# Optimization experiments

Hardware: AMD Instinct MI355X
Metric: run time of the kernel (lower is better)

Reference implementation:

```python
import math
import jax, jax.numpy as jnp
import numpy as np

B, CH3, T = 64, 192, 2048  # B = batch*heads, CH3 = 3*head_dim

def setup_inputs() -> dict:
    key = jax.random.key(0)
    qkv = jax.random.normal(key, (B, CH3, T), dtype=jnp.float32)
    return {"qkv": qkv}

def reference(qkv):
    ch = qkv.shape[1] // 3
    q, k, v = jnp.split(qkv, 3, axis=1)  # each [B, ch, T]
    scale = 1.0 / math.sqrt(math.sqrt(ch))
    # scores [B, T(query), S(key)]
    weight = jnp.einsum('bct,bcs->bts', q * scale, k * scale)
    weight = jax.nn.softmax(weight.astype(jnp.float32), axis=-1).astype(weight.dtype)
    return jnp.einsum('bts,bcs->bct', weight, v)
```

## Files before the change

### kernel.cpp

```cpp
#include <hip/hip_runtime.h>
#include <hip/hip_bf16.h>


#define DHEAD 64
#define TLEN  2048
#define NB    64
#define BQ    256
#define BK    64
#define LDA   72
#define LDT   65

typedef short s16x8 __attribute__((ext_vector_type(8)));
typedef float f32x4 __attribute__((ext_vector_type(4)));
typedef unsigned short u16x4 __attribute__((ext_vector_type(4)));
typedef unsigned short u16x8 __attribute__((ext_vector_type(8)));

__device__ __forceinline__ unsigned short f2bf(float f) {
    unsigned int u = __float_as_uint(f);
    u += 0x7fffu + ((u >> 16) & 1u);
    return (unsigned short)(u >> 16);
}

__device__ __forceinline__ unsigned int cvt_pk_bf16(float a, float b) {
    return (unsigned int)f2bf(a) | ((unsigned int)f2bf(b) << 16);
}

__global__ __launch_bounds__(256)
void prep_qk(const float* __restrict__ qkv, unsigned short* __restrict__ ws) {
    __shared__ float T32[64 * LDT];
    const int tile = blockIdx.x, tensor = blockIdx.y, b = blockIdx.z;
    const int tid = threadIdx.x;
    const float* src = qkv + ((size_t)b * 3 + tensor) * DHEAD * TLEN + tile * 64;
    unsigned short* dst = ws + (size_t)tensor * NB * DHEAD * TLEN
                        + (size_t)b * DHEAD * TLEN + (size_t)tile * 64 * DHEAD;
    {
        int c = tid >> 4, t4 = (tid & 15) * 4;
        #pragma unroll
        for (int rr = 0; rr < 4; ++rr, c += 16) {
            float4 f = *(const float4*)(src + c * TLEN + t4);
            T32[(t4 + 0) * LDT + c] = f.x;
            T32[(t4 + 1) * LDT + c] = f.y;
            T32[(t4 + 2) * LDT + c] = f.z;
            T32[(t4 + 3) * LDT + c] = f.w;
        }
    }
    __syncthreads();
    #pragma unroll
    for (int rep = 0; rep < 2; ++rep) {
        int idx = rep * 256 + tid;
        int t = idx >> 3, j = idx & 7;
        const float* row = &T32[t * LDT + j * 8];
        union { u16x8 v; unsigned int u[4]; } o;
        o.u[0] = cvt_pk_bf16(row[0], row[1]);
        o.u[1] = cvt_pk_bf16(row[2], row[3]);
        o.u[2] = cvt_pk_bf16(row[4], row[5]);
        o.u[3] = cvt_pk_bf16(row[6], row[7]);
        *(u16x8*)(dst + t * DHEAD + j * 8) = o.v;
    }
}

__global__ __launch_bounds__(256)
void prep_v(const float* __restrict__ qkv, unsigned short* __restrict__ ws) {
    const int tile = blockIdx.x, b = blockIdx.y;
    const int tid = threadIdx.x;
    const float* src = qkv + ((size_t)b * 3 + 2) * DHEAD * TLEN + tile * 256;
    unsigned short* dst = ws + (size_t)2 * NB * DHEAD * TLEN
                        + (size_t)b * DHEAD * TLEN + tile * 256;
    int c = tid >> 5, t8 = (tid & 31) * 8;
    #pragma unroll
    for (int rr = 0; rr < 8; ++rr, c += 8) {
        float4 f0 = *(const float4*)(src + c * TLEN + t8);
        float4 f1 = *(const float4*)(src + c * TLEN + t8 + 4);
        union { u16x8 v; unsigned int u[4]; } o;
        o.u[0] = cvt_pk_bf16(f0.x, f0.y);
        o.u[1] = cvt_pk_bf16(f0.z, f0.w);
        o.u[2] = cvt_pk_bf16(f1.x, f1.y);
        o.u[3] = cvt_pk_bf16(f1.z, f1.w);
        *(u16x8*)(dst + c * TLEN + t8) = o.v;
    }
}

__device__ __forceinline__ void loadkv(const unsigned short* kt, const unsigned short* vd,
                                       int s0, u16x8 kc[2], u16x8 vc[2], int tid) {
    #pragma unroll
    for (int r = 0; r < 2; ++r) {
        int id = tid + r * 256;
        kc[r] = *(const u16x8*)(kt + (size_t)s0 * DHEAD + id * 8);
        vc[r] = *(const u16x8*)(vd + (size_t)(id >> 3) * TLEN + s0 + (id & 7) * 8);
    }
}

__device__ __forceinline__ void stage(unsigned short* K, unsigned short* V,
                                      const u16x8 kc[2], const u16x8 vc[2], int tid) {
    #pragma unroll
    for (int r = 0; r < 2; ++r) {
        int id = tid + r * 256;
        *(u16x8*)(&K[(id >> 3) * LDA + (id & 7) * 8]) = kc[r];
        *(u16x8*)(&V[(id >> 3) * LDA + (id & 7) * 8]) = vc[r];
    }
}

__device__ __forceinline__ void compute_tile(const unsigned short* Ks, const unsigned short* Vs,
                                             unsigned short* Pw,
                                             const s16x8 (&qf)[4][2], f32x4 (&acco)[4][4],
                                             float (&lp)[4], int quad, int c16) {
    f32x4 accs[4][4];
    #pragma unroll
    for (int i = 0; i < 4; ++i)
        #pragma unroll
        for (int j = 0; j < 4; ++j) accs[i][j] = f32x4{0.f, 0.f, 0.f, 0.f};
    #pragma unroll
    for (int kk = 0; kk < 2; ++kk)
        #pragma unroll
        for (int st = 0; st < 4; ++st) {
            s16x8 ka = *(const s16x8*)(&Ks[(st * 16 + c16) * LDA + kk * 32 + quad * 8]);
            #pragma unroll
            for (int ts = 0; ts < 4; ++ts)
                accs[st][ts] = __builtin_amdgcn_mfma_f32_16x16x32_bf16(ka, qf[ts][kk], accs[st][ts], 0, 0, 0);
        }

    #pragma unroll
    for (int st = 0; st < 4; ++st)
        #pragma unroll
        for (int ts = 0; ts < 4; ++ts) {
            f32x4 v = accs[st][ts];
            float e0 = __expf(v[0] * 0.125f);
            float e1 = __expf(v[1] * 0.125f);
            float e2 = __expf(v[2] * 0.125f);
            float e3 = __expf(v[3] * 0.125f);
            lp[ts] += (e0 + e1) + (e2 + e3);
            union { u16x4 v4; unsigned int u[2]; } p;
            p.u[0] = cvt_pk_bf16(e0, e1);
            p.u[1] = cvt_pk_bf16(e2, e3);
            *(u16x4*)(&Pw[(ts * 16 + c16) * LDA + st * 16 + quad * 4]) = p.v4;
        }

    #pragma unroll
    for (int kk = 0; kk < 2; ++kk) {
        s16x8 pb[4];
        #pragma unroll
        for (int ts = 0; ts < 4; ++ts)
            pb[ts] = *(const s16x8*)(&Pw[(ts * 16 + c16) * LDA + kk * 32 + quad * 8]);
        #pragma unroll
        for (int cst = 0; cst < 4; ++cst) {
            s16x8 va = *(const s16x8*)(&Vs[(cst * 16 + c16) * LDA + kk * 32 + quad * 8]);
            #pragma unroll
            for (int ts = 0; ts < 4; ++ts)
                acco[cst][ts] = __builtin_amdgcn_mfma_f32_16x16x32_bf16(va, pb[ts], acco[cst][ts], 0, 0, 0);
        }
    }
}

__global__ __launch_bounds__(256, 2)
void attn(const unsigned short* __restrict__ ws, float* __restrict__ out) {
    __shared__ alignas(16) unsigned short Ks2[2][64 * LDA];
    __shared__ alignas(16) unsigned short Vs2[2][64 * LDA];
    __shared__ alignas(16) unsigned short Pt[4][64 * LDA];

    const int tid  = threadIdx.x;
    const int wave = tid >> 6;
    const int lane = tid & 63;
    const int quad = lane >> 4;
    const int c16  = lane & 15;

    const int b  = blockIdx.y;
    const int t0 = blockIdx.x * BQ;

    const unsigned short* qt = ws + (size_t)b * DHEAD * TLEN + (size_t)(t0 + wave * 64) * DHEAD;
    const unsigned short* kt = ws + (size_t)NB * DHEAD * TLEN + (size_t)b * DHEAD * TLEN;
    const unsigned short* vd = ws + (size_t)2 * NB * DHEAD * TLEN + (size_t)b * DHEAD * TLEN;

    s16x8 qf[4][2];
    #pragma unroll
    for (int ts = 0; ts < 4; ++ts)
        #pragma unroll
        for (int kk = 0; kk < 2; ++kk)
            qf[ts][kk] = *(const s16x8*)(qt + (size_t)(ts * 16 + c16) * DHEAD + kk * 32 + quad * 8);

    f32x4 acco[4][4];
    #pragma unroll
    for (int i = 0; i < 4; ++i)
        #pragma unroll
        for (int j = 0; j < 4; ++j) acco[i][j] = f32x4{0.f, 0.f, 0.f, 0.f};
    float lp[4] = {0.f, 0.f, 0.f, 0.f};

    unsigned short* Pw = Pt[wave];

    u16x8 kcA[2], vcA[2], kcB[2], vcB[2];
    loadkv(kt, vd, 0, kcA, vcA, tid);
    loadkv(kt, vd, BK, kcB, vcB, tid);

    for (int it = 0; it < TLEN / BK; it += 2) {
        stage(Ks2[0], Vs2[0], kcA, vcA, tid);
        __syncthreads();
        if (it + 2 < TLEN / BK) loadkv(kt, vd, (it + 2) * BK, kcA, vcA, tid);
        compute_tile(Ks2[0], Vs2[0], Pw, qf, acco, lp, quad, c16);

        stage(Ks2[1], Vs2[1], kcB, vcB, tid);
        __syncthreads();
        if (it + 3 < TLEN / BK) loadkv(kt, vd, (it + 3) * BK, kcB, vcB, tid);
        compute_tile(Ks2[1], Vs2[1], Pw, qf, acco, lp, quad, c16);
    }

    float rinv[4];
    #pragma unroll
    for (int ts = 0; ts < 4; ++ts) {
        float l = lp[ts];
        l += __shfl_xor(l, 16);
        l += __shfl_xor(l, 32);
        rinv[ts] = 1.0f / l;
    }

    float* ob = out + (size_t)b * DHEAD * TLEN + t0 + wave * 64;
    #pragma unroll
    for (int cst = 0; cst < 4; ++cst)
        #pragma unroll
        for (int ts = 0; ts < 4; ++ts)
            #pragma unroll
            for (int r = 0; r < 4; ++r)
                ob[(size_t)(cst * 16 + quad * 4 + r) * TLEN + ts * 16 + c16] = acco[cst][ts][r] * rinv[ts];
}

extern "C" void kernel_launch(void* const* d_in, const int* in_sizes, int n_in,
                              void* d_out, int out_size, void* d_ws, size_t ws_size,
                              hipStream_t stream) {
    const float* qkv = (const float*)d_in[0];
    unsigned short* ws = (unsigned short*)d_ws;
    float* out = (float*)d_out;
    prep_qk<<<dim3(TLEN / 64, 2, NB), 256, 0, stream>>>(qkv, ws);
    prep_v<<<dim3(TLEN / 256, NB), 256, 0, stream>>>(qkv, ws);
    attn<<<dim3(TLEN / BQ, NB), 256, 0, stream>>>(ws, out);
}
```

Baseline: 271.6 us.

## Switch attention to fp16 MFMA with pre-scaled Q/K and single-buffered LDS

Converts the workspace and MFMA operands from bf16 to fp16, using the hardware pkrtz conversion in place of the software round-to-nearest bf16 routine. The score scale is folded into Q and K during prep so the per-element multiply before exp disappears. The attention loop drops the double-buffered K/V LDS tiles for a single buffer with an extra barrier per tile, which shrinks LDS use but exposes more synchronisation. fp16 carries less range than bf16, and the exp values are not max-subtracted, so large scores risk overflowing.

```diff
diff --git a/kernel.cpp b/kernel.cpp
--- a/kernel.cpp
+++ b/kernel.cpp
@@ -1,5 +1,4 @@
 #include <hip/hip_runtime.h>
-#include <hip/hip_bf16.h>
 
 
 #define DHEAD 64
@@ -10,29 +9,28 @@
 #define LDA   72
 #define LDT   65
 
-typedef short s16x8 __attribute__((ext_vector_type(8)));
+typedef _Float16 h16x8 __attribute__((ext_vector_type(8)));
+typedef _Float16 h16x4 __attribute__((ext_vector_type(4)));
+typedef _Float16 h16x2 __attribute__((ext_vector_type(2)));
+typedef __fp16   fp16x2 __attribute__((ext_vector_type(2)));
 typedef float f32x4 __attribute__((ext_vector_type(4)));
-typedef unsigned short u16x4 __attribute__((ext_vector_type(4)));
-typedef unsigned short u16x8 __attribute__((ext_vector_type(8)));
-
-__device__ __forceinline__ unsigned short f2bf(float f) {
-    unsigned int u = __float_as_uint(f);
-    u += 0x7fffu + ((u >> 16) & 1u);
-    return (unsigned short)(u >> 16);
-}
-
-__device__ __forceinline__ unsigned int cvt_pk_bf16(float a, float b) {
-    return (unsigned int)f2bf(a) | ((unsigned int)f2bf(b) << 16);
+
+#define QK_SCALE 0.35355339059327373f
+
+__device__ __forceinline__ h16x2 pkrtz(float a, float b) {
+    union { fp16x2 f; h16x2 h; } u;
+    u.f = __builtin_amdgcn_cvt_pkrtz(a, b);
+    return u.h;
 }
 
 __global__ __launch_bounds__(256)
-void prep_qk(const float* __restrict__ qkv, unsigned short* __restrict__ ws) {
+void prep_qk(const float* __restrict__ qkv, _Float16* __restrict__ ws) {
     __shared__ float T32[64 * LDT];
     const int tile = blockIdx.x, tensor = blockIdx.y, b = blockIdx.z;
     const int tid = threadIdx.x;
     const float* src = qkv + ((size_t)b * 3 + tensor) * DHEAD * TLEN + tile * 64;
-    unsigned short* dst = ws + (size_t)tensor * NB * DHEAD * TLEN
-                        + (size_t)b * DHEAD * TLEN + (size_t)tile * 64 * DHEAD;
+    _Float16* dst = ws + (size_t)tensor * NB * DHEAD * TLEN
+                  + (size_t)b * DHEAD * TLEN + (size_t)tile * 64 * DHEAD;
     {
         int c = tid >> 4, t4 = (tid & 15) * 4;
         #pragma unroll
@@ -50,112 +48,41 @@
         int idx = rep * 256 + tid;
         int t = idx >> 3, j = idx & 7;
         const float* row = &T32[t * LDT + j * 8];
-        union { u16x8 v; unsigned int u[4]; } o;
-        o.u[0] = cvt_pk_bf16(row[0], row[1]);
-        o.u[1] = cvt_pk_bf16(row[2], row[3]);
-        o.u[2] = cvt_pk_bf16(row[4], row[5]);
-        o.u[3] = cvt_pk_bf16(row[6], row[7]);
-        *(u16x8*)(dst + t * DHEAD + j * 8) = o.v;
+        union { h16x8 v; h16x2 h[4]; } o;
+        o.h[0] = pkrtz(row[0] * QK_SCALE, row[1] * QK_SCALE);
+        o.h[1] = pkrtz(row[2] * QK_SCALE, row[3] * QK_SCALE);
+        o.h[2] = pkrtz(row[4] * QK_SCALE, row[5] * QK_SCALE);
+        o.h[3] = pkrtz(row[6] * QK_SCALE, row[7] * QK_SCALE);
+        *(h16x8*)(dst + t * DHEAD + j * 8) = o.v;
     }
 }
 
 __global__ __launch_bounds__(256)
-void prep_v(const float* __restrict__ qkv, unsigned short* __restrict__ ws) {
+void prep_v(const float* __restrict__ qkv, _Float16* __restrict__ ws) {
     const int tile = blockIdx.x, b = blockIdx.y;
     const int tid = threadIdx.x;
     const float* src = qkv + ((size_t)b * 3 + 2) * DHEAD * TLEN + tile * 256;
-    unsigned short* dst = ws + (size_t)2 * NB * DHEAD * TLEN
-                        + (size_t)b * DHEAD * TLEN + tile * 256;
+    _Float16* dst = ws + (size_t)2 * NB * DHEAD * TLEN
+                  + (size_t)b * DHEAD * TLEN + tile * 256;
     int c = tid >> 5, t8 = (tid & 31) * 8;
     #pragma unroll
     for (int rr = 0; rr < 8; ++rr, c += 8) {
         float4 f0 = *(const float4*)(src + c * TLEN + t8);
         float4 f1 = *(const float4*)(src + c * TLEN + t8 + 4);
-        union { u16x8 v; unsigned int u[4]; } o;
-        o.u[0] = cvt_pk_bf16(f0.x, f0.y);
-        o.u[1] = cvt_pk_bf16(f0.z, f0.w);
-        o.u[2] = cvt_pk_bf16(f1.x, f1.y);
-        o.u[3] = cvt_pk_bf16(f1.z, f1.w);
-        *(u16x8*)(dst + c * TLEN + t8) = o.v;
-    }
-}
-
-__device__ __forceinline__ void loadkv(const unsigned short* kt, const unsigned short* vd,
-                                       int s0, u16x8 kc[2], u16x8 vc[2], int tid) {
-    #pragma unroll
-    for (int r = 0; r < 2; ++r) {
-        int id = tid + r * 256;
-        kc[r] = *(const u16x8*)(kt + (size_t)s0 * DHEAD + id * 8);
-        vc[r] = *(const u16x8*)(vd + (size_t)(id >> 3) * TLEN + s0 + (id & 7) * 8);
-    }
-}
-
-__device__ __forceinline__ void stage(unsigned short* K, unsigned short* V,
-                                      const u16x8 kc[2], const u16x8 vc[2], int tid) {
-    #pragma unroll
-    for (int r = 0; r < 2; ++r) {
-        int id = tid + r * 256;
-        *(u16x8*)(&K[(id >> 3) * LDA + (id & 7) * 8]) = kc[r];
-        *(u16x8*)(&V[(id >> 3) * LDA + (id & 7) * 8]) = vc[r];
-    }
-}
-
-__device__ __forceinline__ void compute_tile(const unsigned short* Ks, const unsigned short* Vs,
-                                             unsigned short* Pw,
-                                             const s16x8 (&qf)[4][2], f32x4 (&acco)[4][4],
-                                             float (&lp)[4], int quad, int c16) {
-    f32x4 accs[4][4];
-    #pragma unroll
-    for (int i = 0; i < 4; ++i)
-        #pragma unroll
-        for (int j = 0; j < 4; ++j) accs[i][j] = f32x4{0.f, 0.f, 0.f, 0.f};
-    #pragma unroll
-    for (int kk = 0; kk < 2; ++kk)
-        #pragma unroll
-        for (int st = 0; st < 4; ++st) {
-            s16x8 ka = *(const s16x8*)(&Ks[(st * 16 + c16) * LDA + kk * 32 + quad * 8]);
-            #pragma unroll
-            for (int ts = 0; ts < 4; ++ts)
-                accs[st][ts] = __builtin_amdgcn_mfma_f32_16x16x32_bf16(ka, qf[ts][kk], accs[st][ts], 0, 0, 0);
-        }
-
-    #pragma unroll
-    for (int st = 0; st < 4; ++st)
-        #pragma unroll
-        for (int ts = 0; ts < 4; ++ts) {
-            f32x4 v = accs[st][ts];
-            float e0 = __expf(v[0] * 0.125f);
-            float e1 = __expf(v[1] * 0.125f);
-            float e2 = __expf(v[2] * 0.125f);
-            float e3 = __expf(v[3] * 0.125f);
-            lp[ts] += (e0 + e1) + (e2 + e3);
-            union { u16x4 v4; unsigned int u[2]; } p;
-            p.u[0] = cvt_pk_bf16(e0, e1);
-            p.u[1] = cvt_pk_bf16(e2, e3);
-            *(u16x4*)(&Pw[(ts * 16 + c16) * LDA + st * 16 + quad * 4]) = p.v4;
-        }
-
-    #pragma unroll
-    for (int kk = 0; kk < 2; ++kk) {
-        s16x8 pb[4];
-        #pragma unroll
-        for (int ts = 0; ts < 4; ++ts)
-            pb[ts] = *(const s16x8*)(&Pw[(ts * 16 + c16) * LDA + kk * 32 + quad * 8]);
-        #pragma unroll
-        for (int cst = 0; cst < 4; ++cst) {
-            s16x8 va = *(const s16x8*)(&Vs[(cst * 16 + c16) * LDA + kk * 32 + quad * 8]);
-            #pragma unroll
-            for (int ts = 0; ts < 4; ++ts)
-                acco[cst][ts] = __builtin_amdgcn_mfma_f32_16x16x32_bf16(va, pb[ts], acco[cst][ts], 0, 0, 0);
-        }
+        union { h16x8 v; h16x2 h[4]; } o;
+        o.h[0] = pkrtz(f0.x, f0.y);
+        o.h[1] = pkrtz(f0.z, f0.w);
+        o.h[2] = pkrtz(f1.x, f1.y);
+        o.h[3] = pkrtz(f1.z, f1.w);
+        *(h16x8*)(dst + c * TLEN + t8) = o.v;
     }
 }
 
 __global__ __launch_bounds__(256, 2)
-void attn(const unsigned short* __restrict__ ws, float* __restrict__ out) {
-    __shared__ alignas(16) unsigned short Ks2[2][64 * LDA];
-    __shared__ alignas(16) unsigned short Vs2[2][64 * LDA];
-    __shared__ alignas(16) unsigned short Pt[4][64 * LDA];
+void attn(const _Float16* __restrict__ ws, float* __restrict__ out) {
+    __shared__ alignas(16) _Float16 Ks[64 * LDA];
+    __shared__ alignas(16) _Float16 Vs[64 * LDA];
+    __shared__ alignas(16) _Float16 Pt[4][64 * LDA];
 
     const int tid  = threadIdx.x;
     const int wave = tid >> 6;
@@ -166,16 +93,16 @@
     const int b  = blockIdx.y;
     const int t0 = blockIdx.x * BQ;
 
-    const unsigned short* qt = ws + (size_t)b * DHEAD * TLEN + (size_t)(t0 + wave * 64) * DHEAD;
-    const unsigned short* kt = ws + (size_t)NB * DHEAD * TLEN + (size_t)b * DHEAD * TLEN;
-    const unsigned short* vd = ws + (size_t)2 * NB * DHEAD * TLEN + (size_t)b * DHEAD * TLEN;
-
-    s16x8 qf[4][2];
+    const _Float16* qt = ws + (size_t)b * DHEAD * TLEN + (size_t)(t0 + wave * 64) * DHEAD;
+    const _Float16* kt = ws + (size_t)NB * DHEAD * TLEN + (size_t)b * DHEAD * TLEN;
+    const _Float16* vd = ws + (size_t)2 * NB * DHEAD * TLEN + (size_t)b * DHEAD * TLEN;
+
+    h16x8 qf[4][2];
     #pragma unroll
     for (int ts = 0; ts < 4; ++ts)
         #pragma unroll
         for (int kk = 0; kk < 2; ++kk)
-            qf[ts][kk] = *(const s16x8*)(qt + (size_t)(ts * 16 + c16) * DHEAD + kk * 32 + quad * 8);
+            qf[ts][kk] = *(const h16x8*)(qt + (size_t)(ts * 16 + c16) * DHEAD + kk * 32 + quad * 8);
 
     f32x4 acco[4][4];
     #pragma unroll
@@ -184,22 +111,81 @@
         for (int j = 0; j < 4; ++j) acco[i][j] = f32x4{0.f, 0.f, 0.f, 0.f};
     float lp[4] = {0.f, 0.f, 0.f, 0.f};
 
-    unsigned short* Pw = Pt[wave];
-
-    u16x8 kcA[2], vcA[2], kcB[2], vcB[2];
-    loadkv(kt, vd, 0, kcA, vcA, tid);
-    loadkv(kt, vd, BK, kcB, vcB, tid);
-
-    for (int it = 0; it < TLEN / BK; it += 2) {
-        stage(Ks2[0], Vs2[0], kcA, vcA, tid);
+    _Float16* Pw = Pt[wave];
+
+    h16x8 kc[2], vc[2];
+    #pragma unroll
+    for (int r = 0; r < 2; ++r) {
+        int id = tid + r * 256;
+        kc[r] = *(const h16x8*)(kt + (size_t)id * 8);
+        vc[r] = *(const h16x8*)(vd + (size_t)(id >> 3) * TLEN + (id & 7) * 8);
+    }
+
+    for (int it = 0; it < TLEN / BK; ++it) {
         __syncthreads();
-        if (it + 2 < TLEN / BK) loadkv(kt, vd, (it + 2) * BK, kcA, vcA, tid);
-        compute_tile(Ks2[0], Vs2[0], Pw, qf, acco, lp, quad, c16);
-
-        stage(Ks2[1], Vs2[1], kcB, vcB, tid);
+        #pragma unroll
+        for (int r = 0; r < 2; ++r) {
+            int id = tid + r * 256;
+            *(h16x8*)(&Ks[(id >> 3) * LDA + (id & 7) * 8]) = kc[r];
+            *(h16x8*)(&Vs[(id >> 3) * LDA + (id & 7) * 8]) = vc[r];
+        }
         __syncthreads();
-        if (it + 3 < TLEN / BK) loadkv(kt, vd, (it + 3) * BK, kcB, vcB, tid);
-        compute_tile(Ks2[1], Vs2[1], Pw, qf, acco, lp, quad, c16);
+
+        if (it + 1 < TLEN / BK) {
+            int s0 = (it + 1) * BK;
+            #pragma unroll
+            for (int r = 0; r < 2; ++r) {
+                int id = tid + r * 256;
+                kc[r] = *(const h16x8*)(kt + (size_t)s0 * DHEAD + id * 8);
+                vc[r] = *(const h16x8*)(vd + (size_t)(id >> 3) * TLEN + s0 + (id & 7) * 8);
+            }
+        }
+
+        f32x4 accs[4][4];
+        #pragma unroll
+        for (int i = 0; i < 4; ++i)
+            #pragma unroll
+            for (int j = 0; j < 4; ++j) accs[i][j] = f32x4{0.f, 0.f, 0.f, 0.f};
+        #pragma unroll
+        for (int kk = 0; kk < 2; ++kk)
+            #pragma unroll
+            for (int st = 0; st < 4; ++st) {
+                h16x8 ka = *(const h16x8*)(&Ks[(st * 16 + c16) * LDA + kk * 32 + quad * 8]);
+                #pragma unroll
+                for (int ts = 0; ts < 4; ++ts)
+                    accs[st][ts] = __builtin_amdgcn_mfma_f32_16x16x32_f16(ka, qf[ts][kk], accs[st][ts], 0, 0, 0);
+            }
+
+        #pragma unroll
+        for (int st = 0; st < 4; ++st)
+            #pragma unroll
+            for (int ts = 0; ts < 4; ++ts) {
+                f32x4 v = accs[st][ts];
+                float e0 = __expf(v[0]);
+                float e1 = __expf(v[1]);
+                float e2 = __expf(v[2]);
+                float e3 = __expf(v[3]);
+                lp[ts] += (e0 + e1) + (e2 + e3);
+                union { h16x4 v4; h16x2 h[2]; } p;
+                p.h[0] = pkrtz(e0, e1);
+                p.h[1] = pkrtz(e2, e3);
+                *(h16x4*)(&Pw[(ts * 16 + c16) * LDA + st * 16 + quad * 4]) = p.v4;
+            }
+
+        #pragma unroll
+        for (int kk = 0; kk < 2; ++kk) {
+            h16x8 pb[4];
+            #pragma unroll
+            for (int ts = 0; ts < 4; ++ts)
+                pb[ts] = *(const h16x8*)(&Pw[(ts * 16 + c16) * LDA + kk * 32 + quad * 8]);
+            #pragma unroll
+            for (int cst = 0; cst < 4; ++cst) {
+                h16x8 va = *(const h16x8*)(&Vs[(cst * 16 + c16) * LDA + kk * 32 + quad * 8]);
+                #pragma unroll
+                for (int ts = 0; ts < 4; ++ts)
+                    acco[cst][ts] = __builtin_amdgcn_mfma_f32_16x16x32_f16(va, pb[ts], acco[cst][ts], 0, 0, 0);
+            }
+        }
     }
 
     float rinv[4];
@@ -225,7 +211,7 @@
                               void* d_out, int out_size, void* d_ws, size_t ws_size,
                               hipStream_t stream) {
     const float* qkv = (const float*)d_in[0];
-    unsigned short* ws = (unsigned short*)d_ws;
+    _Float16* ws = (_Float16*)d_ws;
     float* out = (float*)d_out;
     prep_qk<<<dim3(TLEN / 64, 2, NB), 256, 0, stream>>>(qkv, ws);
     prep_v<<<dim3(TLEN / 256, NB), 256, 0, stream>>>(qkv, ws);
```

After: 242.6 us. -10.7%, faster.
